# Kernel optimization log

Measured on AMD Instinct MI355X. Metric: run time of the kernel, lower is better.

The kernel has to match this reference:

```python
import jax, jax.numpy as jnp
import numpy as np

B, T, D, A = 16, 2048, 512, 64


def setup_inputs() -> dict:
    key = jax.random.key(0)
    ks = jax.random.split(key, 7)
    s = 1.0 / np.sqrt(D)
    return {
        "inp": jax.random.normal(ks[0], (B, T, D), dtype=jnp.float32),
        "Wq": jax.random.normal(ks[1], (D, A), dtype=jnp.float32) * s,
        "bq": jax.random.normal(ks[2], (A,), dtype=jnp.float32) * 0.01,
        "Wk": jax.random.normal(ks[3], (D, A), dtype=jnp.float32) * s,
        "bk": jax.random.normal(ks[4], (A,), dtype=jnp.float32) * 0.01,
        "Wv": jax.random.normal(ks[5], (D, A), dtype=jnp.float32) * s,
        "bv": jax.random.normal(ks[6], (A,), dtype=jnp.float32) * 0.01,
    }


def reference(inp, Wq, bq, Wk, bk, Wv, bv):
    # Projections: (B,T,D) @ (D,A) -> (B,T,A)
    Q = inp @ Wq + bq
    K = inp @ Wk + bk
    V = inp @ Wv + bv
    # Scaled QK^T: (B,T,T)
    scores = jnp.einsum("btd,bsd->bts", Q, K) / jnp.sqrt(jnp.float32(A))
    # Sign-based K padding mask: mask[b, s] = sign(|sum_a K[b,s,a]|)
    k_mask = jnp.sign(jnp.abs(K.sum(axis=-1)))  # (B,T)
    scores = jnp.where(k_mask[:, None, :] == 0, jnp.float32(1e-8), scores)
    att = jax.nn.softmax(scores, axis=-1)
    # Sign-based Q mask broadcast along the key axis (faithful to Mask module)
    q_mask = jnp.sign(jnp.abs(Q.sum(axis=-1)))  # (B,T)
    att = att * q_mask[:, None, :]
    # dropout_keep_prob == 1 -> dropout is identity
    ctx = jnp.einsum("bts,bsa->bta", att, V)  # (B,T,A)
    # inp^T @ ctx -> (B,D,A), then sum over A -> (B,D)
    out = jnp.einsum("btd,bta->bd", inp, ctx)
    return out
```

## Files before the change

### kernel.cpp

```cpp
#include <hip/hip_runtime.h>

#define B_ 16
#define T_ 2048
#define D_ 512
#define SCALE_LOG2E 0.18033688f

typedef __bf16 bf16x8 __attribute__((ext_vector_type(8)));
typedef float  f32x4  __attribute__((ext_vector_type(4)));

__device__ inline unsigned short f2bf(float f){
    union { float f; unsigned u; } x; x.f = f;
    unsigned r = x.u + 0x7fffu + ((x.u >> 16) & 1u);
    return (unsigned short)(r >> 16);
}

__device__ inline bf16x8 ldfrag(const unsigned short* p){
    uint4 v = *reinterpret_cast<const uint4*>(p);
    return __builtin_bit_cast(bf16x8, v);
}


__global__ void setup_kernel(const float* __restrict__ Wq, const float* __restrict__ Wk,
                             const float* __restrict__ Wv, const float* __restrict__ bq,
                             const float* __restrict__ bk, const float* __restrict__ bv,
                             unsigned short* __restrict__ WcT, float* __restrict__ bsum,
                             float* __restrict__ numden, float* __restrict__ out)
{
    int e = blockIdx.x * 256 + threadIdx.x;
    if (e < 73728){
        int j = e >> 9, d = e & 511;
        float v;
        if (j < 64)       v = Wq[d * 64 + j];
        else if (j < 128) v = Wk[d * 64 + (j - 64)];
        else if (j < 131){
            const float* src = (j == 128) ? Wq : (j == 129) ? Wk : Wv;
            const float4* p = reinterpret_cast<const float4*>(&src[d * 64]);
            v = 0.f;
            #pragma unroll
            for (int i = 0; i < 16; i++){ float4 t = p[i]; v += (t.x + t.y) + (t.z + t.w); }
        }
        else v = 0.f;
        WcT[j * 512 + d] = f2bf(v);
    } else if (e < 73744){
        int mm = e - 73728;
        float s = 0.f;
        const float* src = (mm == 0) ? bq : (mm == 1) ? bk : bv;
        if (mm < 3){
            const float4* p = reinterpret_cast<const float4*>(src);
            #pragma unroll
            for (int i = 0; i < 16; i++){ float4 t = p[i]; s += (t.x + t.y) + (t.z + t.w); }
        }
        bsum[mm] = s;
    } else if (e < 139280){
        numden[e - 73744] = 0.f;
    } else if (e < 147472){
        out[e - 139280] = 0.f;
    }
}

__global__ __launch_bounds__(256) void proj_kernel(
    const float* __restrict__ inp, const unsigned short* __restrict__ WcT,
    const float* __restrict__ bq, const float* __restrict__ bk,
    const float* __restrict__ bsum,
    unsigned short* __restrict__ Qb, unsigned short* __restrict__ Kb,
    float* __restrict__ wvp)
{
    __shared__ __align__(16) unsigned short Af[4 * 512];
    __shared__ __align__(16) unsigned short Bf[9 * 512];
    __shared__ float kzsh[64];
    const int tid  = threadIdx.x;
    const int r0   = blockIdx.x * 64;
    const int lane = tid & 63, wvid = tid >> 6;
    const int m = lane & 15, q = lane >> 4;
    const int mh = wvid >> 1, nh = wvid & 1;

    const int ar = tid >> 2, aseg = tid & 3;
    unsigned short* a_dst = &Af[(ar >> 4) * 512 + (aseg * 16 + (ar & 15)) * 8];
    const float* a_src = &inp[(size_t)(r0 + ar) * 512 + aseg * 8];
    const unsigned short* b_src0 = &WcT[(((tid      ) >> 6) * 16 + (tid & 15)) * 512 + ((tid >> 4) & 3) * 8];
    const unsigned short* b_src1 = &WcT[(((tid + 256) >> 6) * 16 + (tid & 15)) * 512 + ((tid >> 4) & 3) * 8];
    const unsigned short* b_src2 = &WcT[(((tid + 512) >> 6) * 16 + (tid & 15)) * 512 + ((tid >> 4) & 3) * 8];
    uint4* b_dst0 = reinterpret_cast<uint4*>(&Bf[(tid      ) * 8]);
    uint4* b_dst1 = reinterpret_cast<uint4*>(&Bf[(tid + 256) * 8]);
    uint4* b_dst2 = reinterpret_cast<uint4*>(&Bf[(tid + 512) * 8]);

    f32x4 acc[5][2];
    #pragma unroll
    for (int t = 0; t < 5; t++){
        acc[t][0] = (f32x4){0.f, 0.f, 0.f, 0.f};
        acc[t][1] = (f32x4){0.f, 0.f, 0.f, 0.f};
    }

    float4 ga0 = *reinterpret_cast<const float4*>(a_src);
    float4 ga1 = *reinterpret_cast<const float4*>(a_src + 4);
    uint4 gb0 = *reinterpret_cast<const uint4*>(b_src0);
    uint4 gb1 = *reinterpret_cast<const uint4*>(b_src1);
    uint4 gb2 = (tid < 64) ? *reinterpret_cast<const uint4*>(b_src2) : (uint4){0,0,0,0};

    const int ntile = 5 - nh;
    const int tbase = nh * 5;

    for (int kk = 0; kk < 512; kk += 32){
        uint4 pk;
        pk.x = f2bf(ga0.x) | ((unsigned)f2bf(ga0.y) << 16);
        pk.y = f2bf(ga0.z) | ((unsigned)f2bf(ga0.w) << 16);
        pk.z = f2bf(ga1.x) | ((unsigned)f2bf(ga1.y) << 16);
        pk.w = f2bf(ga1.z) | ((unsigned)f2bf(ga1.w) << 16);
        *reinterpret_cast<uint4*>(a_dst) = pk;
        *b_dst0 = gb0;
        *b_dst1 = gb1;
        if (tid < 64) *b_dst2 = gb2;
        __syncthreads();
        if (kk < 480){
            ga0 = *reinterpret_cast<const float4*>(a_src + kk + 32);
            ga1 = *reinterpret_cast<const float4*>(a_src + kk + 36);
            gb0 = *reinterpret_cast<const uint4*>(b_src0 + kk + 32);
            gb1 = *reinterpret_cast<const uint4*>(b_src1 + kk + 32);
            if (tid < 64) gb2 = *reinterpret_cast<const uint4*>(b_src2 + kk + 32);
        }
        bf16x8 a0 = ldfrag(&Af[(mh * 2    ) * 512 + lane * 8]);
        bf16x8 a1 = ldfrag(&Af[(mh * 2 + 1) * 512 + lane * 8]);
        #pragma unroll
        for (int t = 0; t < 5; t++){
            if (t < ntile){
                bf16x8 bfr = ldfrag(&Bf[(tbase + t) * 512 + lane * 8]);
                acc[t][0] = __builtin_amdgcn_mfma_f32_16x16x32_bf16(a0, bfr, acc[t][0], 0, 0, 0);
                acc[t][1] = __builtin_amdgcn_mfma_f32_16x16x32_bf16(a1, bfr, acc[t][1], 0, 0, 0);
            }
        }
        __syncthreads();
    }

    if (nh == 1){
        const float bs = bsum[m];
        #pragma unroll
        for (int f = 0; f < 2; f++){
            #pragma unroll
            for (int i = 0; i < 4; i++){
                int rl = mh * 32 + f * 16 + q * 4 + i;
                float val = acc[3][f][i] + bs;
                float qsv = __shfl(val, (lane & 48));
                float ksv = __shfl(val, (lane & 48) | 1);
                float vsv = __shfl(val, (lane & 48) | 2);
                if (m == 0){
                    kzsh[rl] = (ksv == 0.f) ? 0.f : 1.f;
                    wvp[(size_t)r0 + rl] = (qsv == 0.f) ? 0.f : vsv;
                }
            }
        }
    }
    __syncthreads();

    if (nh == 0){
        float bqv[4];
        #pragma unroll
        for (int t = 0; t < 4; t++) bqv[t] = bq[t * 16 + m];
        const float bkv0 = bk[m];
        #pragma unroll
        for (int f = 0; f < 2; f++){
            #pragma unroll
            for (int i = 0; i < 4; i++){
                int rl = mh * 32 + f * 16 + q * 4 + i;
                size_t r = (size_t)r0 + rl;
                float kz = kzsh[rl];
                #pragma unroll
                for (int t = 0; t < 4; t++)
                    Qb[r * 64 + t * 16 + m] = f2bf((acc[t][f][i] + bqv[t]) * SCALE_LOG2E);
                Kb[r * 64 + m] = f2bf((acc[4][f][i] + bkv0) * kz);
            }
        }
    } else {
        float bkv[3];
        #pragma unroll
        for (int t = 0; t < 3; t++) bkv[t] = bk[16 + t * 16 + m];
        #pragma unroll
        for (int f = 0; f < 2; f++){
            #pragma unroll
            for (int i = 0; i < 4; i++){
                int rl = mh * 32 + f * 16 + q * 4 + i;
                size_t r = (size_t)r0 + rl;
                float kz = kzsh[rl];
                #pragma unroll
                for (int t = 0; t < 3; t++)
                    Kb[r * 64 + 16 + t * 16 + m] = f2bf((acc[t][f][i] + bkv[t]) * kz);
            }
        }
    }
}

__global__ __launch_bounds__(512) void attn_kernel(
    const unsigned short* __restrict__ Qb, const unsigned short* __restrict__ Kb,
    const float* __restrict__ wvp, float* __restrict__ num_g, float* __restrict__ den_g)
{
    __shared__ __align__(16) unsigned short Kf[8 * 512];
    const int tid = threadIdx.x;
    const int lane = tid & 63, wvid = tid >> 6;
    const int m = lane & 15, q = lane >> 4;
    const int b  = blockIdx.y;
    const int t0 = blockIdx.x * 256 + wvid * 32;
    const int s0 = blockIdx.z * 512;
    const size_t base = (size_t)b * T_;

    const unsigned short* qp = &Qb[(base + t0 + m) * 64 + q * 8];
    bf16x8 a00 = ldfrag(qp),            a01 = ldfrag(qp + 32);
    bf16x8 a10 = ldfrag(qp + 16 * 64),  a11 = ldfrag(qp + 16 * 64 + 32);

    const unsigned short* ksrc = &Kb[(base + s0 + (wvid >> 1) * 16 + m) * 64 + (wvid & 1) * 32 + q * 8];
    uint4* kdst = reinterpret_cast<uint4*>(&Kf[wvid * 512 + lane * 8]);
    uint4 stg = *reinterpret_cast<const uint4*>(ksrc);

    float num0[4] = {0,0,0,0}, den0[4] = {0,0,0,0};
    float num1[4] = {0,0,0,0}, den1[4] = {0,0,0,0};

    for (int it = 0; it < 8; it++){
        *kdst = stg;
        __syncthreads();
        if (it < 7) stg = *reinterpret_cast<const uint4*>(ksrc + (it + 1) * 64 * 64);
        float w[4];
        #pragma unroll
        for (int st = 0; st < 4; st++) w[st] = wvp[base + s0 + it * 64 + st * 16 + m];
        #pragma unroll
        for (int st = 0; st < 4; st++){
            bf16x8 b0 = ldfrag(&Kf[(st * 2    ) * 512 + lane * 8]);
            bf16x8 b1 = ldfrag(&Kf[(st * 2 + 1) * 512 + lane * 8]);
            f32x4 z0 = (f32x4){0.f,0.f,0.f,0.f};
            z0 = __builtin_amdgcn_mfma_f32_16x16x32_bf16(a00, b0, z0, 0, 0, 0);
            z0 = __builtin_amdgcn_mfma_f32_16x16x32_bf16(a01, b1, z0, 0, 0, 0);
            f32x4 z1 = (f32x4){0.f,0.f,0.f,0.f};
            z1 = __builtin_amdgcn_mfma_f32_16x16x32_bf16(a10, b0, z1, 0, 0, 0);
            z1 = __builtin_amdgcn_mfma_f32_16x16x32_bf16(a11, b1, z1, 0, 0, 0);
            float wst = w[st];
            #pragma unroll
            for (int i = 0; i < 4; i++){
                float e0 = exp2f(z0[i]);
                den0[i] += e0; num0[i] = fmaf(e0, wst, num0[i]);
                float e1 = exp2f(z1[i]);
                den1[i] += e1; num1[i] = fmaf(e1, wst, num1[i]);
            }
        }
        __syncthreads();
    }
    #pragma unroll
    for (int s = 1; s < 16; s <<= 1){
        #pragma unroll
        for (int i = 0; i < 4; i++){
            num0[i] += __shfl_xor(num0[i], s); den0[i] += __shfl_xor(den0[i], s);
            num1[i] += __shfl_xor(num1[i], s); den1[i] += __shfl_xor(den1[i], s);
        }
    }
    if (m == 0){
        #pragma unroll
        for (int i = 0; i < 4; i++){
            atomicAdd(&num_g[base + t0 + q * 4 + i],      num0[i]);
            atomicAdd(&den_g[base + t0 + q * 4 + i],      den0[i]);
            atomicAdd(&num_g[base + t0 + 16 + q * 4 + i], num1[i]);
            atomicAdd(&den_g[base + t0 + 16 + q * 4 + i], den1[i]);
        }
    }
}

__global__ __launch_bounds__(256) void out_kernel(
    const float* __restrict__ inp, const float* __restrict__ num_g,
    const float* __restrict__ den_g, float* __restrict__ out)
{
    __shared__ float csh[32];
    const int tid = threadIdx.x;
    const int b   = blockIdx.y;
    const int t0  = blockIdx.x * 32;
    const size_t base = (size_t)b * T_;
    if (tid < 32) csh[tid] = num_g[base + t0 + tid] / den_g[base + t0 + tid];
    __syncthreads();
    const float2* ip = reinterpret_cast<const float2*>(inp + (base + t0) * 512);
    float a0 = 0.f, a1 = 0.f;
    #pragma unroll 8
    for (int t = 0; t < 32; t++){
        float ct = csh[t];
        float2 v = ip[(size_t)t * 256 + tid];
        a0 = fmaf(v.x, ct, a0);
        a1 = fmaf(v.y, ct, a1);
    }
    atomicAdd(&out[b * 512 + 2 * tid],     a0);
    atomicAdd(&out[b * 512 + 2 * tid + 1], a1);
}

extern "C" void kernel_launch(void* const* d_in, const int* in_sizes, int n_in,
                              void* d_out, int out_size, void* d_ws, size_t ws_size,
                              hipStream_t stream)
{
    const float* inp = (const float*)d_in[0];
    const float* Wq  = (const float*)d_in[1];
    const float* bq  = (const float*)d_in[2];
    const float* Wk  = (const float*)d_in[3];
    const float* bk  = (const float*)d_in[4];
    const float* Wv  = (const float*)d_in[5];
    const float* bv  = (const float*)d_in[6];
    float* out = (float*)d_out;

    char* ws = (char*)d_ws;
    unsigned short* WcT = (unsigned short*)(ws);
    float* bsum         = (float*)(ws + 147456);
    unsigned short* Qb  = (unsigned short*)(ws + 262144);
    unsigned short* Kb  = (unsigned short*)(ws + 4456448);
    float* wvp          = (float*)(ws + 8650752);
    float* num_g        = (float*)(ws + 8781824);
    float* den_g        = (float*)(ws + 8912896);

    setup_kernel<<<577, 256, 0, stream>>>(Wq, Wk, Wv, bq, bk, bv, WcT, bsum, num_g, out);
    proj_kernel<<<512, 256, 0, stream>>>(inp, WcT, bq, bk, bsum, Qb, Kb, wvp);
    attn_kernel<<<dim3(8, 16, 4), 512, 0, stream>>>(Qb, Kb, wvp, num_g, den_g);
    out_kernel<<<dim3(64, 16), 256, 0, stream>>>(inp, num_g, den_g, out);
}
```

Measured before the change: 154.5 us.

## Double-buffer LDS tiles and replace atomic partial sums with per-split buffers

The LDS tiles in the projection and attention kernels become double-buffered. This removes the trailing barrier in each loop iteration, so the next tile's stores can overlap with the current compute. The attention kernel's atomicAdd reductions of num/den across the 4 key splits are replaced by plain stores into per-split buffers, which the output kernel sums. This also removes the need to zero num/den in setup. The cost is twice the shared memory and four extra loads per row in out_kernel.

```diff
diff --git a/kernel.cpp b/kernel.cpp
--- a/kernel.cpp
+++ b/kernel.cpp
@@ -24,7 +24,7 @@
                              const float* __restrict__ Wv, const float* __restrict__ bq,
                              const float* __restrict__ bk, const float* __restrict__ bv,
                              unsigned short* __restrict__ WcT, float* __restrict__ bsum,
-                             float* __restrict__ numden, float* __restrict__ out)
+                             float* __restrict__ out)
 {
     int e = blockIdx.x * 256 + threadIdx.x;
     if (e < 73728){
@@ -51,10 +51,8 @@
             for (int i = 0; i < 16; i++){ float4 t = p[i]; s += (t.x + t.y) + (t.z + t.w); }
         }
         bsum[mm] = s;
-    } else if (e < 139280){
-        numden[e - 73744] = 0.f;
-    } else if (e < 147472){
-        out[e - 139280] = 0.f;
+    } else if (e < 81936){
+        out[e - 73744] = 0.f;
     }
 }
 
@@ -65,8 +63,8 @@
     unsigned short* __restrict__ Qb, unsigned short* __restrict__ Kb,
     float* __restrict__ wvp)
 {
-    __shared__ __align__(16) unsigned short Af[4 * 512];
-    __shared__ __align__(16) unsigned short Bf[9 * 512];
+    __shared__ __align__(16) unsigned short Af[2][4 * 512];
+    __shared__ __align__(16) unsigned short Bf[2][9 * 512];
     __shared__ float kzsh[64];
     const int tid  = threadIdx.x;
     const int r0   = blockIdx.x * 64;
@@ -75,14 +73,12 @@
     const int mh = wvid >> 1, nh = wvid & 1;
 
     const int ar = tid >> 2, aseg = tid & 3;
-    unsigned short* a_dst = &Af[(ar >> 4) * 512 + (aseg * 16 + (ar & 15)) * 8];
+    const int a_off = (ar >> 4) * 512 + (aseg * 16 + (ar & 15)) * 8;
     const float* a_src = &inp[(size_t)(r0 + ar) * 512 + aseg * 8];
     const unsigned short* b_src0 = &WcT[(((tid      ) >> 6) * 16 + (tid & 15)) * 512 + ((tid >> 4) & 3) * 8];
     const unsigned short* b_src1 = &WcT[(((tid + 256) >> 6) * 16 + (tid & 15)) * 512 + ((tid >> 4) & 3) * 8];
     const unsigned short* b_src2 = &WcT[(((tid + 512) >> 6) * 16 + (tid & 15)) * 512 + ((tid >> 4) & 3) * 8];
-    uint4* b_dst0 = reinterpret_cast<uint4*>(&Bf[(tid      ) * 8]);
-    uint4* b_dst1 = reinterpret_cast<uint4*>(&Bf[(tid + 256) * 8]);
-    uint4* b_dst2 = reinterpret_cast<uint4*>(&Bf[(tid + 512) * 8]);
+    const int b_off0 = tid * 8, b_off1 = (tid + 256) * 8, b_off2 = (tid + 512) * 8;
 
     f32x4 acc[5][2];
     #pragma unroll
@@ -100,36 +96,40 @@
     const int ntile = 5 - nh;
     const int tbase = nh * 5;
 
-    for (int kk = 0; kk < 512; kk += 32){
+    for (int it = 0; it < 16; it++){
+        const int p = it & 1;
+        unsigned short* Ab = Af[p];
+        unsigned short* Bb = Bf[p];
         uint4 pk;
         pk.x = f2bf(ga0.x) | ((unsigned)f2bf(ga0.y) << 16);
         pk.y = f2bf(ga0.z) | ((unsigned)f2bf(ga0.w) << 16);
         pk.z = f2bf(ga1.x) | ((unsigned)f2bf(ga1.y) << 16);
         pk.w = f2bf(ga1.z) | ((unsigned)f2bf(ga1.w) << 16);
-        *reinterpret_cast<uint4*>(a_dst) = pk;
-        *b_dst0 = gb0;
-        *b_dst1 = gb1;
-        if (tid < 64) *b_dst2 = gb2;
+        *reinterpret_cast<uint4*>(&Ab[a_off]) = pk;
+        *reinterpret_cast<uint4*>(&Bb[b_off0]) = gb0;
+        *reinterpret_cast<uint4*>(&Bb[b_off1]) = gb1;
+        if (tid < 64) *reinterpret_cast<uint4*>(&Bb[b_off2]) = gb2;
         __syncthreads();
-        if (kk < 480){
-            ga0 = *reinterpret_cast<const float4*>(a_src + kk + 32);
-            ga1 = *reinterpret_cast<const float4*>(a_src + kk + 36);
-            gb0 = *reinterpret_cast<const uint4*>(b_src0 + kk + 32);
-            gb1 = *reinterpret_cast<const uint4*>(b_src1 + kk + 32);
-            if (tid < 64) gb2 = *reinterpret_cast<const uint4*>(b_src2 + kk + 32);
-        }
-        bf16x8 a0 = ldfrag(&Af[(mh * 2    ) * 512 + lane * 8]);
-        bf16x8 a1 = ldfrag(&Af[(mh * 2 + 1) * 512 + lane * 8]);
+        if (it < 15){
+            const int kn = (it + 1) * 32;
+            ga0 = *reinterpret_cast<const float4*>(a_src + kn);
+            ga1 = *reinterpret_cast<const float4*>(a_src + kn + 4);
+            gb0 = *reinterpret_cast<const uint4*>(b_src0 + kn);
+            gb1 = *reinterpret_cast<const uint4*>(b_src1 + kn);
+            if (tid < 64) gb2 = *reinterpret_cast<const uint4*>(b_src2 + kn);
+        }
+        bf16x8 a0 = ldfrag(&Ab[(mh * 2    ) * 512 + lane * 8]);
+        bf16x8 a1 = ldfrag(&Ab[(mh * 2 + 1) * 512 + lane * 8]);
         #pragma unroll
         for (int t = 0; t < 5; t++){
             if (t < ntile){
-                bf16x8 bfr = ldfrag(&Bf[(tbase + t) * 512 + lane * 8]);
+                bf16x8 bfr = ldfrag(&Bb[(tbase + t) * 512 + lane * 8]);
                 acc[t][0] = __builtin_amdgcn_mfma_f32_16x16x32_bf16(a0, bfr, acc[t][0], 0, 0, 0);
                 acc[t][1] = __builtin_amdgcn_mfma_f32_16x16x32_bf16(a1, bfr, acc[t][1], 0, 0, 0);
             }
         }
-        __syncthreads();
-    }
+    }
+    __syncthreads();
 
     if (nh == 1){
         const float bs = bsum[m];
@@ -190,9 +190,9 @@
 
 __global__ __launch_bounds__(512) void attn_kernel(
     const unsigned short* __restrict__ Qb, const unsigned short* __restrict__ Kb,
-    const float* __restrict__ wvp, float* __restrict__ num_g, float* __restrict__ den_g)
-{
-    __shared__ __align__(16) unsigned short Kf[8 * 512];
+    const float* __restrict__ wvp, float* __restrict__ num_s, float* __restrict__ den_s)
+{
+    __shared__ __align__(16) unsigned short Kf[2][8 * 512];
     const int tid = threadIdx.x;
     const int lane = tid & 63, wvid = tid >> 6;
     const int m = lane & 15, q = lane >> 4;
@@ -200,20 +200,22 @@
     const int t0 = blockIdx.x * 256 + wvid * 32;
     const int s0 = blockIdx.z * 512;
     const size_t base = (size_t)b * T_;
+    const size_t zoff = (size_t)blockIdx.z * (B_ * T_);
 
     const unsigned short* qp = &Qb[(base + t0 + m) * 64 + q * 8];
     bf16x8 a00 = ldfrag(qp),            a01 = ldfrag(qp + 32);
     bf16x8 a10 = ldfrag(qp + 16 * 64),  a11 = ldfrag(qp + 16 * 64 + 32);
 
     const unsigned short* ksrc = &Kb[(base + s0 + (wvid >> 1) * 16 + m) * 64 + (wvid & 1) * 32 + q * 8];
-    uint4* kdst = reinterpret_cast<uint4*>(&Kf[wvid * 512 + lane * 8]);
+    const int k_off = wvid * 512 + lane * 8;
     uint4 stg = *reinterpret_cast<const uint4*>(ksrc);
 
     float num0[4] = {0,0,0,0}, den0[4] = {0,0,0,0};
     float num1[4] = {0,0,0,0}, den1[4] = {0,0,0,0};
 
     for (int it = 0; it < 8; it++){
-        *kdst = stg;
+        const int p = it & 1;
+        *reinterpret_cast<uint4*>(&Kf[p][k_off]) = stg;
         __syncthreads();
         if (it < 7) stg = *reinterpret_cast<const uint4*>(ksrc + (it + 1) * 64 * 64);
         float w[4];
@@ -221,8 +223,8 @@
         for (int st = 0; st < 4; st++) w[st] = wvp[base + s0 + it * 64 + st * 16 + m];
         #pragma unroll
         for (int st = 0; st < 4; st++){
-            bf16x8 b0 = ldfrag(&Kf[(st * 2    ) * 512 + lane * 8]);
-            bf16x8 b1 = ldfrag(&Kf[(st * 2 + 1) * 512 + lane * 8]);
+            bf16x8 b0 = ldfrag(&Kf[p][(st * 2    ) * 512 + lane * 8]);
+            bf16x8 b1 = ldfrag(&Kf[p][(st * 2 + 1) * 512 + lane * 8]);
             f32x4 z0 = (f32x4){0.f,0.f,0.f,0.f};
             z0 = __builtin_amdgcn_mfma_f32_16x16x32_bf16(a00, b0, z0, 0, 0, 0);
             z0 = __builtin_amdgcn_mfma_f32_16x16x32_bf16(a01, b1, z0, 0, 0, 0);
@@ -238,7 +240,6 @@
                 den1[i] += e1; num1[i] = fmaf(e1, wst, num1[i]);
             }
         }
-        __syncthreads();
     }
     #pragma unroll
     for (int s = 1; s < 16; s <<= 1){
@@ -251,24 +252,29 @@
     if (m == 0){
         #pragma unroll
         for (int i = 0; i < 4; i++){
-            atomicAdd(&num_g[base + t0 + q * 4 + i],      num0[i]);
-            atomicAdd(&den_g[base + t0 + q * 4 + i],      den0[i]);
-            atomicAdd(&num_g[base + t0 + 16 + q * 4 + i], num1[i]);
-            atomicAdd(&den_g[base + t0 + 16 + q * 4 + i], den1[i]);
+            num_s[zoff + base + t0 + q * 4 + i]      = num0[i];
+            den_s[zoff + base + t0 + q * 4 + i]      = den0[i];
+            num_s[zoff + base + t0 + 16 + q * 4 + i] = num1[i];
+            den_s[zoff + base + t0 + 16 + q * 4 + i] = den1[i];
         }
     }
 }
 
 __global__ __launch_bounds__(256) void out_kernel(
-    const float* __restrict__ inp, const float* __restrict__ num_g,
-    const float* __restrict__ den_g, float* __restrict__ out)
+    const float* __restrict__ inp, const float* __restrict__ num_s,
+    const float* __restrict__ den_s, float* __restrict__ out)
 {
     __shared__ float csh[32];
     const int tid = threadIdx.x;
     const int b   = blockIdx.y;
     const int t0  = blockIdx.x * 32;
     const size_t base = (size_t)b * T_;
-    if (tid < 32) csh[tid] = num_g[base + t0 + tid] / den_g[base + t0 + tid];
+    if (tid < 32){
+        size_t idx = base + t0 + tid;
+        float n = num_s[idx] + num_s[32768 + idx] + num_s[65536 + idx] + num_s[98304 + idx];
+        float d = den_s[idx] + den_s[32768 + idx] + den_s[65536 + idx] + den_s[98304 + idx];
+        csh[tid] = n / d;
+    }
     __syncthreads();
     const float2* ip = reinterpret_cast<const float2*>(inp + (base + t0) * 512);
     float a0 = 0.f, a1 = 0.f;
@@ -302,11 +308,11 @@
     unsigned short* Qb  = (unsigned short*)(ws + 262144);
     unsigned short* Kb  = (unsigned short*)(ws + 4456448);
     float* wvp          = (float*)(ws + 8650752);
-    float* num_g        = (float*)(ws + 8781824);
-    float* den_g        = (float*)(ws + 8912896);
-
-    setup_kernel<<<577, 256, 0, stream>>>(Wq, Wk, Wv, bq, bk, bv, WcT, bsum, num_g, out);
+    float* num_s        = (float*)(ws + 8781824);
+    float* den_s        = (float*)(ws + 9306112);
+
+    setup_kernel<<<321, 256, 0, stream>>>(Wq, Wk, Wv, bq, bk, bv, WcT, bsum, out);
     proj_kernel<<<512, 256, 0, stream>>>(inp, WcT, bq, bk, bsum, Qb, Kb, wvp);
-    attn_kernel<<<dim3(8, 16, 4), 512, 0, stream>>>(Qb, Kb, wvp, num_g, den_g);
-    out_kernel<<<dim3(64, 16), 256, 0, stream>>>(inp, num_g, den_g, out);
-}
+    attn_kernel<<<dim3(8, 16, 4), 512, 0, stream>>>(Qb, Kb, wvp, num_s, den_s);
+    out_kernel<<<dim3(64, 16), 256, 0, stream>>>(inp, num_s, den_s, out);
+}
```

New measurement: 156.7 us. No clear change (+1.5%).

## Fuse attention and output reduction into one kernel with double-buffered K tiles

Applied to the files above, without the earlier changes.

The attention and output kernels are merged. Each block now owns 128 query rows and loops over the full key length, so num/den are finished in-block and no global atomics or zero-initialisation for them are needed. The block then multiplies the resulting context weights straight against inp. K tiles are double-buffered in shared memory, which drops one barrier per iteration. The trade-off is that the grid shrinks from 512 blocks to 256, each doing a longer serial loop over keys, and each wave now handles 16 rows instead of 32, so there is less MFMA reuse per K fragment.

```diff
diff --git a/kernel.cpp b/kernel.cpp
--- a/kernel.cpp
+++ b/kernel.cpp
@@ -24,7 +24,7 @@
                              const float* __restrict__ Wv, const float* __restrict__ bq,
                              const float* __restrict__ bk, const float* __restrict__ bv,
                              unsigned short* __restrict__ WcT, float* __restrict__ bsum,
-                             float* __restrict__ numden, float* __restrict__ out)
+                             float* __restrict__ out)
 {
     int e = blockIdx.x * 256 + threadIdx.x;
     if (e < 73728){
@@ -51,10 +51,8 @@
             for (int i = 0; i < 16; i++){ float4 t = p[i]; s += (t.x + t.y) + (t.z + t.w); }
         }
         bsum[mm] = s;
-    } else if (e < 139280){
-        numden[e - 73744] = 0.f;
-    } else if (e < 147472){
-        out[e - 139280] = 0.f;
+    } else if (e < 81936){
+        out[e - 73744] = 0.f;
     }
 }
 
@@ -188,99 +186,75 @@
     }
 }
 
-__global__ __launch_bounds__(512) void attn_kernel(
+__global__ __launch_bounds__(512) void attn_out_kernel(
+    const float* __restrict__ inp,
     const unsigned short* __restrict__ Qb, const unsigned short* __restrict__ Kb,
-    const float* __restrict__ wvp, float* __restrict__ num_g, float* __restrict__ den_g)
-{
-    __shared__ __align__(16) unsigned short Kf[8 * 512];
+    const float* __restrict__ wvp, float* __restrict__ out)
+{
+    __shared__ __align__(16) unsigned short Kf[2][8 * 512];
+    __shared__ float csh[128];
     const int tid = threadIdx.x;
     const int lane = tid & 63, wvid = tid >> 6;
     const int m = lane & 15, q = lane >> 4;
     const int b  = blockIdx.y;
-    const int t0 = blockIdx.x * 256 + wvid * 32;
-    const int s0 = blockIdx.z * 512;
+    const int t0 = blockIdx.x * 128;
     const size_t base = (size_t)b * T_;
 
-    const unsigned short* qp = &Qb[(base + t0 + m) * 64 + q * 8];
-    bf16x8 a00 = ldfrag(qp),            a01 = ldfrag(qp + 32);
-    bf16x8 a10 = ldfrag(qp + 16 * 64),  a11 = ldfrag(qp + 16 * 64 + 32);
-
-    const unsigned short* ksrc = &Kb[(base + s0 + (wvid >> 1) * 16 + m) * 64 + (wvid & 1) * 32 + q * 8];
-    uint4* kdst = reinterpret_cast<uint4*>(&Kf[wvid * 512 + lane * 8]);
+    const unsigned short* qp = &Qb[(base + t0 + wvid * 16 + m) * 64 + q * 8];
+    bf16x8 a0 = ldfrag(qp), a1 = ldfrag(qp + 32);
+
+    const unsigned short* ksrc = &Kb[(base + (wvid >> 1) * 16 + m) * 64 + (wvid & 1) * 32 + q * 8];
+    const int k_off = wvid * 512 + lane * 8;
     uint4 stg = *reinterpret_cast<const uint4*>(ksrc);
 
-    float num0[4] = {0,0,0,0}, den0[4] = {0,0,0,0};
-    float num1[4] = {0,0,0,0}, den1[4] = {0,0,0,0};
-
-    for (int it = 0; it < 8; it++){
-        *kdst = stg;
+    float num[4] = {0,0,0,0}, den[4] = {0,0,0,0};
+
+    for (int it = 0; it < 32; it++){
+        const int p = it & 1;
+        *reinterpret_cast<uint4*>(&Kf[p][k_off]) = stg;
         __syncthreads();
-        if (it < 7) stg = *reinterpret_cast<const uint4*>(ksrc + (it + 1) * 64 * 64);
+        if (it < 31) stg = *reinterpret_cast<const uint4*>(ksrc + (it + 1) * 4096);
         float w[4];
         #pragma unroll
-        for (int st = 0; st < 4; st++) w[st] = wvp[base + s0 + it * 64 + st * 16 + m];
+        for (int st = 0; st < 4; st++) w[st] = wvp[base + it * 64 + st * 16 + m];
         #pragma unroll
         for (int st = 0; st < 4; st++){
-            bf16x8 b0 = ldfrag(&Kf[(st * 2    ) * 512 + lane * 8]);
-            bf16x8 b1 = ldfrag(&Kf[(st * 2 + 1) * 512 + lane * 8]);
-            f32x4 z0 = (f32x4){0.f,0.f,0.f,0.f};
-            z0 = __builtin_amdgcn_mfma_f32_16x16x32_bf16(a00, b0, z0, 0, 0, 0);
-            z0 = __builtin_amdgcn_mfma_f32_16x16x32_bf16(a01, b1, z0, 0, 0, 0);
-            f32x4 z1 = (f32x4){0.f,0.f,0.f,0.f};
-            z1 = __builtin_amdgcn_mfma_f32_16x16x32_bf16(a10, b0, z1, 0, 0, 0);
-            z1 = __builtin_amdgcn_mfma_f32_16x16x32_bf16(a11, b1, z1, 0, 0, 0);
+            bf16x8 b0 = ldfrag(&Kf[p][(st * 2    ) * 512 + lane * 8]);
+            bf16x8 b1 = ldfrag(&Kf[p][(st * 2 + 1) * 512 + lane * 8]);
+            f32x4 z = (f32x4){0.f,0.f,0.f,0.f};
+            z = __builtin_amdgcn_mfma_f32_16x16x32_bf16(a0, b0, z, 0, 0, 0);
+            z = __builtin_amdgcn_mfma_f32_16x16x32_bf16(a1, b1, z, 0, 0, 0);
             float wst = w[st];
             #pragma unroll
             for (int i = 0; i < 4; i++){
-                float e0 = exp2f(z0[i]);
-                den0[i] += e0; num0[i] = fmaf(e0, wst, num0[i]);
-                float e1 = exp2f(z1[i]);
-                den1[i] += e1; num1[i] = fmaf(e1, wst, num1[i]);
-            }
-        }
-        __syncthreads();
+                float e = exp2f(z[i]);
+                den[i] += e;
+                num[i] = fmaf(e, wst, num[i]);
+            }
+        }
     }
     #pragma unroll
     for (int s = 1; s < 16; s <<= 1){
         #pragma unroll
         for (int i = 0; i < 4; i++){
-            num0[i] += __shfl_xor(num0[i], s); den0[i] += __shfl_xor(den0[i], s);
-            num1[i] += __shfl_xor(num1[i], s); den1[i] += __shfl_xor(den1[i], s);
-        }
-    }
+            num[i] += __shfl_xor(num[i], s);
+            den[i] += __shfl_xor(den[i], s);
+        }
+    }
+    __syncthreads();
     if (m == 0){
         #pragma unroll
-        for (int i = 0; i < 4; i++){
-            atomicAdd(&num_g[base + t0 + q * 4 + i],      num0[i]);
-            atomicAdd(&den_g[base + t0 + q * 4 + i],      den0[i]);
-            atomicAdd(&num_g[base + t0 + 16 + q * 4 + i], num1[i]);
-            atomicAdd(&den_g[base + t0 + 16 + q * 4 + i], den1[i]);
-        }
-    }
-}
-
-__global__ __launch_bounds__(256) void out_kernel(
-    const float* __restrict__ inp, const float* __restrict__ num_g,
-    const float* __restrict__ den_g, float* __restrict__ out)
-{
-    __shared__ float csh[32];
-    const int tid = threadIdx.x;
-    const int b   = blockIdx.y;
-    const int t0  = blockIdx.x * 32;
-    const size_t base = (size_t)b * T_;
-    if (tid < 32) csh[tid] = num_g[base + t0 + tid] / den_g[base + t0 + tid];
+        for (int i = 0; i < 4; i++)
+            csh[wvid * 16 + q * 4 + i] = num[i] / den[i];
+    }
     __syncthreads();
-    const float2* ip = reinterpret_cast<const float2*>(inp + (base + t0) * 512);
-    float a0 = 0.f, a1 = 0.f;
+
+    const float* ip = inp + (base + t0) * 512 + tid;
+    float a = 0.f;
     #pragma unroll 8
-    for (int t = 0; t < 32; t++){
-        float ct = csh[t];
-        float2 v = ip[(size_t)t * 256 + tid];
-        a0 = fmaf(v.x, ct, a0);
-        a1 = fmaf(v.y, ct, a1);
-    }
-    atomicAdd(&out[b * 512 + 2 * tid],     a0);
-    atomicAdd(&out[b * 512 + 2 * tid + 1], a1);
+    for (int t = 0; t < 128; t++)
+        a = fmaf(ip[(size_t)t * 512], csh[t], a);
+    atomicAdd(&out[b * 512 + tid], a);
 }
 
 extern "C" void kernel_launch(void* const* d_in, const int* in_sizes, int n_in,
@@ -302,11 +276,8 @@
     unsigned short* Qb  = (unsigned short*)(ws + 262144);
     unsigned short* Kb  = (unsigned short*)(ws + 4456448);
     float* wvp          = (float*)(ws + 8650752);
-    float* num_g        = (float*)(ws + 8781824);
-    float* den_g        = (float*)(ws + 8912896);
-
-    setup_kernel<<<577, 256, 0, stream>>>(Wq, Wk, Wv, bq, bk, bv, WcT, bsum, num_g, out);
+
+    setup_kernel<<<321, 256, 0, stream>>>(Wq, Wk, Wv, bq, bk, bv, WcT, bsum, out);
     proj_kernel<<<512, 256, 0, stream>>>(inp, WcT, bq, bk, bsum, Qb, Kb, wvp);
-    attn_kernel<<<dim3(8, 16, 4), 512, 0, stream>>>(Qb, Kb, wvp, num_g, den_g);
-    out_kernel<<<dim3(64, 16), 256, 0, stream>>>(inp, num_g, den_g, out);
-}
+    attn_out_kernel<<<dim3(16, 16), 512, 0, stream>>>(inp, Qb, Kb, wvp, out);
+}
```

Measured after the change: 152.8 us (median of 2 runs). No clear change (-1.1%).
